# Kernel tuning notes

Hardware: AMD Instinct MI355X
Metric: run time of the kernel (lower is better)

The kernel has to match this reference:

```python
import jax, jax.numpy as jnp
import numpy as np

B, L, H, E, M = 4, 4096, 8, 64, 64
IN_CH, OUT_CH = 512, 512
SCALE = 1.0 / (IN_CH * OUT_CH)


def setup_inputs() -> dict:
    key = jax.random.key(0)
    k0, k1, k2, k3, k4 = jax.random.split(key, 5)
    q = jax.random.normal(k0, (B, L, H, E), dtype=jnp.float32)
    k = jax.random.normal(k1, (B, L, H, E), dtype=jnp.float32)
    v = jax.random.normal(k2, (B, L, H, E), dtype=jnp.float32)
    # torch.rand on a complex dtype fills real and imag parts with U[0,1)
    w_real = SCALE * jax.random.uniform(k3, (H, H, E, M), dtype=jnp.float32)
    w_imag = SCALE * jax.random.uniform(k4, (H, H, E, M), dtype=jnp.float32)
    # mode_select_method != 'random' -> lowest M modes, sorted
    index = jnp.arange(M, dtype=jnp.int32)
    mask = 0
    return {"q": q, "k": k, "v": v, "w_real": w_real, "w_imag": w_imag, "index": index, "mask": mask}


def reference(q, k, v, w_real, w_imag, index, mask):
    weights = w_real + 1j * w_imag                      # [H,H,E,M] complex64
    x = jnp.transpose(q, (0, 2, 3, 1))                   # [B,H,E,L]
    x_ft = jnp.fft.rfft(x, axis=-1)                      # [B,H,E,L//2+1]
    xg = jnp.take(x_ft, index, axis=-1)                  # gather selected modes: [B,H,E,M]
    # per-(E, mode) head-mixing: 'bix,iox->box' batched over modes
    res = jnp.einsum('bixm,ioxm->boxm', xg, weights)     # [B,H,E,M]
    Lh = L // 2 + 1
    out_ft = jnp.zeros((B, H, E, Lh), dtype=res.dtype).at[..., :M].set(res)
    x_out = jnp.fft.irfft(out_ft, n=L, axis=-1)          # [B,H,E,L] float32
    return x_out
```

## Files before the change

kernel.cpp:

```cpp
#include <hip/hip_runtime.h>

#define Bsz 4
#define Lsz 4096
#define HEsz 512
#define SPLIT 16

typedef __attribute__((ext_vector_type(8))) short short8;
typedef __attribute__((ext_vector_type(4))) float f32x4;

#define OFF_CF  0u
#define OFF_C1P (1u<<20)

static __device__ __forceinline__ unsigned short f2bf(float f) {
    union { float f; unsigned u; } v; v.f = f;
    unsigned u = v.u;
    return (unsigned short)((u + 0x7fffu + ((u >> 16) & 1u)) >> 16);
}
static __device__ __forceinline__ unsigned pk2(float a, float b) {
    return (unsigned)f2bf(a) | ((unsigned)f2bf(b) << 16);
}
static __device__ __forceinline__ float bf2f(unsigned short u) {
    union { unsigned u; float f; } v; v.u = ((unsigned)u) << 16;
    return v.f;
}
static __device__ __forceinline__ void sc(int m, int l, float* s, float* c) {
    int r = (m * l) & (Lsz - 1);
    float ang = (float)r * (6.283185307179586f / (float)Lsz);
    __sincosf(ang, s, c);
}

__global__ __launch_bounds__(256, 2) void k_dft(const float* __restrict__ q,
                                                unsigned short* __restrict__ C1P) {
    __shared__ unsigned short As[64 * 64];
    __shared__ unsigned short Bs[128 * 64];
    const int ks = blockIdx.x, ht = blockIdx.y, b = blockIdx.z;
    const int he0 = ht * 64;
    const int t = threadIdx.x, lane = t & 63, w = t >> 6;
    const int wtm = w & 1, wtn = w >> 1;
    const int quad = lane >> 4, lid = lane & 15;
    f32x4 acc[2][4] = {};

    const int kbeg = ks * (Lsz / SPLIT);
    for (int ch = 0; ch < 4; ++ch) {
        const int l0 = kbeg + ch * 64;
        {
            const float* qp = q + ((size_t)(b * Lsz + l0 + w * 16) * HEsz + he0 + lane);
            float f[16];
#pragma unroll
            for (int j = 0; j < 16; ++j) f[j] = qp[(size_t)j * HEsz];
            uint4 p0 = make_uint4(pk2(f[0], f[1]), pk2(f[2], f[3]), pk2(f[4], f[5]), pk2(f[6], f[7]));
            uint4 p1 = make_uint4(pk2(f[8], f[9]), pk2(f[10], f[11]), pk2(f[12], f[13]), pk2(f[14], f[15]));
            int row = lane;
            int cb0 = (w * 2) ^ (row & 7), cb1 = (w * 2 + 1) ^ (row & 7);
            *(uint4*)(As + row * 64 + cb0 * 8) = p0;
            *(uint4*)(As + row * 64 + cb1 * 8) = p1;
        }
        {
            int m = t & 63, lg = t >> 6;
            int c0 = 2 * m, c1 = 2 * m + 1;
#pragma unroll
            for (int h = 0; h < 2; ++h) {
                float sv[8], cv[8];
#pragma unroll
                for (int j = 0; j < 8; ++j)
                    sc(m, l0 + lg * 16 + h * 8 + j, &sv[j], &cv[j]);
                uint4 pc = make_uint4(pk2(cv[0], cv[1]), pk2(cv[2], cv[3]),
                                      pk2(cv[4], cv[5]), pk2(cv[6], cv[7]));
                uint4 ps = make_uint4(pk2(-sv[0], -sv[1]), pk2(-sv[2], -sv[3]),
                                      pk2(-sv[4], -sv[5]), pk2(-sv[6], -sv[7]));
                int lb = lg * 2 + h;
                *(uint4*)(Bs + c0 * 64 + ((lb ^ (c0 & 7)) * 8)) = pc;
                *(uint4*)(Bs + c1 * 64 + ((lb ^ (c1 & 7)) * 8)) = ps;
            }
        }
        __syncthreads();
#pragma unroll
        for (int kst = 0; kst < 2; ++kst) {
            short8 af[2], bfr[4];
#pragma unroll
            for (int mt = 0; mt < 2; ++mt) {
                int m = wtm * 32 + mt * 16 + lid;
                int cb = (kst * 4 + quad) ^ (m & 7);
                af[mt] = *(short8*)(As + m * 64 + cb * 8);
            }
#pragma unroll
            for (int nt = 0; nt < 4; ++nt) {
                int n = wtn * 64 + nt * 16 + lid;
                int cb = (kst * 4 + quad) ^ (n & 7);
                bfr[nt] = *(short8*)(Bs + n * 64 + cb * 8);
            }
#pragma unroll
            for (int mt = 0; mt < 2; ++mt)
#pragma unroll
                for (int nt = 0; nt < 4; ++nt)
                    acc[mt][nt] = __builtin_amdgcn_mfma_f32_16x16x32_bf16(af[mt], bfr[nt], acc[mt][nt], 0, 0, 0);
        }
        __syncthreads();
    }
    unsigned short* dst = C1P + (((size_t)ks * Bsz + b) * HEsz + he0) * 128;
#pragma unroll
    for (int mt = 0; mt < 2; ++mt)
#pragma unroll
        for (int nt = 0; nt < 4; ++nt)
#pragma unroll
            for (int r = 0; r < 4; ++r)
                dst[(size_t)(wtm * 32 + mt * 16 + quad * 4 + r) * 128 + wtn * 64 + nt * 16 + lid] =
                    f2bf(acc[mt][nt][r]);
}

__global__ __launch_bounds__(256) void k_mixreduce(const unsigned short* __restrict__ C1P,
                                                   const float* __restrict__ wr,
                                                   const float* __restrict__ wi,
                                                   unsigned short* __restrict__ Cf) {
    __shared__ float X[8][128];
    const int e = blockIdx.x & 63, b = blockIdx.x >> 6;
    const int t = threadIdx.x;
    const int i = t >> 5, c4 = t & 31;
    size_t off = ((size_t)b * HEsz + i * 64 + e) * 128 + c4 * 4;
    float sx = 0.f, sy = 0.f, sz = 0.f, sw = 0.f;
    for (int sp = 0; sp < SPLIT; ++sp) {
        uint2 v = *(const uint2*)(C1P + off + (size_t)sp * (Bsz * HEsz * 128));
        sx += bf2f((unsigned short)(v.x & 0xffff));
        sy += bf2f((unsigned short)(v.x >> 16));
        sz += bf2f((unsigned short)(v.y & 0xffff));
        sw += bf2f((unsigned short)(v.y >> 16));
    }
    *(float4*)&X[i][c4 * 4] = make_float4(sx, sy, sz, sw);
    __syncthreads();
#pragma unroll
    for (int it = 0; it < 2; ++it) {
        int item = t + it * 256;
        int o = item >> 6, m = item & 63;
        float ar = 0.f, ai = 0.f;
#pragma unroll
        for (int i2 = 0; i2 < 8; ++i2) {
            float xr = X[i2][2 * m], xi = X[i2][2 * m + 1];
            size_t wo = ((size_t)(i2 * 8 + o) * 64 + e) * 64 + m;
            float wrv = wr[wo], wiv = wi[wo];
            ar += xr * wrv - xi * wiv;
            ai += xr * wiv + xi * wrv;
        }
        int row = b * HEsz + o * 64 + e;
        *(unsigned*)(Cf + (size_t)row * 128 + 2 * m) = pk2(ar, -ai);
    }
}

__global__ __launch_bounds__(256, 2) void k_idft(const unsigned short* __restrict__ Cf,
                                                 float* __restrict__ out) {
    __shared__ unsigned short As[128 * 128];
    __shared__ unsigned short Bs[128 * 128];
    const int l0 = blockIdx.x * 128, row0 = blockIdx.y * 128;
    const int t = threadIdx.x, lane = t & 63, w = t >> 6;
    const int wtm = w & 1, wtn = w >> 1;
    const int quad = lane >> 4, lid = lane & 15;
#pragma unroll
    for (int it = 0; it < 8; ++it) {
        int slot = t + it * 256;
        int r = slot >> 4, cb = slot & 15;
        uint4 a = *(const uint4*)(Cf + (size_t)(row0 + r) * 128 + cb * 8);
        *(uint4*)(As + r * 128 + ((cb ^ (r & 15)) * 8)) = a;
    }
    {
        int lr = t >> 1, half = t & 1;
        int lg = l0 + lr;
#pragma unroll
        for (int jj = 0; jj < 8; ++jj) {
            unsigned wv[4];
#pragma unroll
            for (int j = 0; j < 4; ++j) {
                int m = half * 32 + jj * 4 + j;
                float s, co; sc(m, lg, &s, &co);
                float wm = (m == 0) ? (1.0f / Lsz) : (2.0f / Lsz);
                wv[j] = pk2(wm * co, wm * s);
            }
            int cb = half * 8 + jj;
            *(uint4*)(Bs + lr * 128 + ((cb ^ (lr & 15)) * 8)) =
                make_uint4(wv[0], wv[1], wv[2], wv[3]);
        }
    }
    __syncthreads();
    f32x4 acc[4][4] = {};
#pragma unroll
    for (int kst = 0; kst < 4; ++kst) {
        short8 af[4], bfr[4];
#pragma unroll
        for (int mt = 0; mt < 4; ++mt) {
            int m = wtm * 64 + mt * 16 + lid;
            int cb = (kst * 4 + quad) ^ (m & 15);
            af[mt] = *(short8*)(As + m * 128 + cb * 8);
        }
#pragma unroll
        for (int nt = 0; nt < 4; ++nt) {
            int n = wtn * 64 + nt * 16 + lid;
            int cb = (kst * 4 + quad) ^ (n & 15);
            bfr[nt] = *(short8*)(Bs + n * 128 + cb * 8);
        }
#pragma unroll
        for (int mt = 0; mt < 4; ++mt)
#pragma unroll
            for (int nt = 0; nt < 4; ++nt)
                acc[mt][nt] = __builtin_amdgcn_mfma_f32_16x16x32_bf16(af[mt], bfr[nt], acc[mt][nt], 0, 0, 0);
    }
    __syncthreads();
    float* outb = (float*)As;
#pragma unroll
    for (int mt = 0; mt < 4; ++mt)
#pragma unroll
        for (int nt = 0; nt < 4; ++nt)
#pragma unroll
            for (int r = 0; r < 4; ++r)
                outb[(size_t)(wtm * 64 + mt * 16 + quad * 4 + r) * 128 + wtn * 64 + nt * 16 + lid] =
                    acc[mt][nt][r];
    __syncthreads();
#pragma unroll
    for (int it = 0; it < 16; ++it) {
        int slot = t + it * 256;
        int r = slot >> 5, c4 = slot & 31;
        float4 v = *(float4*)(outb + (size_t)r * 128 + c4 * 4);
        *(float4*)(out + (size_t)(row0 + r) * Lsz + l0 + c4 * 4) = v;
    }
}

extern "C" void kernel_launch(void* const* d_in, const int* in_sizes, int n_in,
                              void* d_out, int out_size, void* d_ws, size_t ws_size,
                              hipStream_t stream) {
    const float* q      = (const float*)d_in[0];
    const float* w_real = (const float*)d_in[3];
    const float* w_imag = (const float*)d_in[4];
    float* out = (float*)d_out;
    char* ws = (char*)d_ws;

    unsigned short* Cf  = (unsigned short*)(ws + OFF_CF);
    unsigned short* C1P = (unsigned short*)(ws + OFF_C1P);

    k_dft      <<<dim3(SPLIT, 8, 4), 256, 0, stream>>>(q, C1P);
    k_mixreduce<<<256, 256, 0, stream>>>(C1P, w_real, w_imag, Cf);
    k_idft     <<<dim3(32, 16), 256, 0, stream>>>(Cf, out);
}
```

Before: 144.6 us.

## Prefetch q chunks, stage DFT outputs through LDS, swizzle IDFT epilogue

In the DFT kernel, the next 64-row chunk of q is loaded into registers while the current chunk's twiddles and MFMAs are computed. The bf16 results are then staged through shared memory so they can be written back with 16-byte coalesced stores instead of scattered 2-byte stores. The IDFT kernel issues its global loads of Cf before computing twiddles, hiding load latency, and XOR-swizzles the fp32 output staging buffer to reduce LDS bank conflicts. The split-reduction loop in the mixing kernel is unrolled. The prefetch raises register pressure, which may affect occupancy.

```diff
diff --git a/kernel.cpp b/kernel.cpp
--- a/kernel.cpp
+++ b/kernel.cpp
@@ -41,13 +41,15 @@
     f32x4 acc[2][4] = {};
 
     const int kbeg = ks * (Lsz / SPLIT);
+    const float* qp0 = q + ((size_t)(b * Lsz + kbeg + w * 16) * HEsz + he0 + lane);
+
+    float f[16], f2[16];
+#pragma unroll
+    for (int j = 0; j < 16; ++j) f[j] = qp0[(size_t)j * HEsz];
+
+#pragma unroll
     for (int ch = 0; ch < 4; ++ch) {
-        const int l0 = kbeg + ch * 64;
         {
-            const float* qp = q + ((size_t)(b * Lsz + l0 + w * 16) * HEsz + he0 + lane);
-            float f[16];
-#pragma unroll
-            for (int j = 0; j < 16; ++j) f[j] = qp[(size_t)j * HEsz];
             uint4 p0 = make_uint4(pk2(f[0], f[1]), pk2(f[2], f[3]), pk2(f[4], f[5]), pk2(f[6], f[7]));
             uint4 p1 = make_uint4(pk2(f[8], f[9]), pk2(f[10], f[11]), pk2(f[12], f[13]), pk2(f[14], f[15]));
             int row = lane;
@@ -55,9 +57,15 @@
             *(uint4*)(As + row * 64 + cb0 * 8) = p0;
             *(uint4*)(As + row * 64 + cb1 * 8) = p1;
         }
+        if (ch < 3) {
+            const float* qp = qp0 + (size_t)(ch + 1) * 64 * HEsz;
+#pragma unroll
+            for (int j = 0; j < 16; ++j) f2[j] = qp[(size_t)j * HEsz];
+        }
         {
             int m = t & 63, lg = t >> 6;
             int c0 = 2 * m, c1 = 2 * m + 1;
+            const int l0 = kbeg + ch * 64;
 #pragma unroll
             for (int h = 0; h < 2; ++h) {
                 float sv[8], cv[8];
@@ -96,16 +104,32 @@
                     acc[mt][nt] = __builtin_amdgcn_mfma_f32_16x16x32_bf16(af[mt], bfr[nt], acc[mt][nt], 0, 0, 0);
         }
         __syncthreads();
-    }
+        if (ch < 3) {
+#pragma unroll
+            for (int j = 0; j < 16; ++j) f[j] = f2[j];
+        }
+    }
+#pragma unroll
+    for (int mt = 0; mt < 2; ++mt)
+#pragma unroll
+        for (int nt = 0; nt < 4; ++nt) {
+            int col = wtn * 64 + nt * 16 + lid;
+#pragma unroll
+            for (int r = 0; r < 4; ++r) {
+                int row = wtm * 32 + mt * 16 + quad * 4 + r;
+                int cb = (col >> 3) ^ (row & 15);
+                Bs[row * 128 + cb * 8 + (col & 7)] = f2bf(acc[mt][nt][r]);
+            }
+        }
+    __syncthreads();
     unsigned short* dst = C1P + (((size_t)ks * Bsz + b) * HEsz + he0) * 128;
 #pragma unroll
-    for (int mt = 0; mt < 2; ++mt)
-#pragma unroll
-        for (int nt = 0; nt < 4; ++nt)
-#pragma unroll
-            for (int r = 0; r < 4; ++r)
-                dst[(size_t)(wtm * 32 + mt * 16 + quad * 4 + r) * 128 + wtn * 64 + nt * 16 + lid] =
-                    f2bf(acc[mt][nt][r]);
+    for (int it = 0; it < 4; ++it) {
+        int slot = t + it * 256;
+        int r = slot >> 4, cb = slot & 15;
+        *(uint4*)(dst + (size_t)r * 128 + cb * 8) =
+            *(const uint4*)(Bs + r * 128 + ((cb ^ (r & 15)) * 8));
+    }
 }
 
 __global__ __launch_bounds__(256) void k_mixreduce(const unsigned short* __restrict__ C1P,
@@ -118,6 +142,7 @@
     const int i = t >> 5, c4 = t & 31;
     size_t off = ((size_t)b * HEsz + i * 64 + e) * 128 + c4 * 4;
     float sx = 0.f, sy = 0.f, sz = 0.f, sw = 0.f;
+#pragma unroll
     for (int sp = 0; sp < SPLIT; ++sp) {
         uint2 v = *(const uint2*)(C1P + off + (size_t)sp * (Bsz * HEsz * 128));
         sx += bf2f((unsigned short)(v.x & 0xffff));
@@ -153,12 +178,12 @@
     const int t = threadIdx.x, lane = t & 63, w = t >> 6;
     const int wtm = w & 1, wtn = w >> 1;
     const int quad = lane >> 4, lid = lane & 15;
+    uint4 a[8];
 #pragma unroll
     for (int it = 0; it < 8; ++it) {
         int slot = t + it * 256;
         int r = slot >> 4, cb = slot & 15;
-        uint4 a = *(const uint4*)(Cf + (size_t)(row0 + r) * 128 + cb * 8);
-        *(uint4*)(As + r * 128 + ((cb ^ (r & 15)) * 8)) = a;
+        a[it] = *(const uint4*)(Cf + (size_t)(row0 + r) * 128 + cb * 8);
     }
     {
         int lr = t >> 1, half = t & 1;
@@ -178,6 +203,12 @@
                 make_uint4(wv[0], wv[1], wv[2], wv[3]);
         }
     }
+#pragma unroll
+    for (int it = 0; it < 8; ++it) {
+        int slot = t + it * 256;
+        int r = slot >> 4, cb = slot & 15;
+        *(uint4*)(As + r * 128 + ((cb ^ (r & 15)) * 8)) = a[it];
+    }
     __syncthreads();
     f32x4 acc[4][4] = {};
 #pragma unroll
@@ -206,17 +237,21 @@
 #pragma unroll
     for (int mt = 0; mt < 4; ++mt)
 #pragma unroll
-        for (int nt = 0; nt < 4; ++nt)
-#pragma unroll
-            for (int r = 0; r < 4; ++r)
-                outb[(size_t)(wtm * 64 + mt * 16 + quad * 4 + r) * 128 + wtn * 64 + nt * 16 + lid] =
-                    acc[mt][nt][r];
+        for (int nt = 0; nt < 4; ++nt) {
+            int col = wtn * 64 + nt * 16 + lid;
+            int c4 = col >> 2, cr = col & 3;
+#pragma unroll
+            for (int r = 0; r < 4; ++r) {
+                int row = wtm * 64 + mt * 16 + quad * 4 + r;
+                outb[(size_t)row * 128 + ((c4 ^ (row & 7)) << 2) + cr] = acc[mt][nt][r];
+            }
+        }
     __syncthreads();
 #pragma unroll
     for (int it = 0; it < 16; ++it) {
         int slot = t + it * 256;
         int r = slot >> 5, c4 = slot & 31;
-        float4 v = *(float4*)(outb + (size_t)r * 128 + c4 * 4);
+        float4 v = *(float4*)(outb + (size_t)r * 128 + ((c4 ^ (r & 7)) << 2));
         *(float4*)(out + (size_t)(row0 + r) * Lsz + l0 + c4 * 4) = v;
     }
 }
```

After: 144.3 us. Within noise of the previous version (-0.2%).
